# Kernel tuning notes

Measured on AMD Instinct MI355X. Metric: run time of the kernel, lower is better.

## Reference

```python
import jax, jax.numpy as jnp
import numpy as np

M = 128        # out_features (= in_features here)
N = 20000      # num_node
E = 320000     # num edges (avg degree 16)
KAPPA = 0.99   # inf-norm projection radius (A_rho = 1.0)


def project_linf(W, v):
    """Project each row of W onto the L1 ball of radius v (=> ||W||_inf <= v),
    matching IGNN's projection_norm_inf (rows with L1 norm <= v are untouched)."""
    absW = jnp.abs(W)
    row_l1 = absW.sum(axis=1)
    u = jnp.sort(absW, axis=1)[:, ::-1]          # descending per row
    cssv = jnp.cumsum(u, axis=1) - v
    ind = jnp.arange(1, W.shape[1] + 1, dtype=W.dtype)
    rho = jnp.sum(u * ind > cssv, axis=1)        # support size, >=1 when row_l1 > v
    theta = cssv[jnp.arange(W.shape[0]), rho - 1] / rho.astype(W.dtype)
    proj = jnp.sign(W) * jnp.maximum(absW - theta[:, None], 0.0)
    return jnp.where((row_l1 > v)[:, None], proj, W)


def spmm_right(Xm, rows, cols, vals, n):
    """Compute Xm @ A for sparse A with A[rows[e], cols[e]] = vals[e]; Xm: [m, n]."""
    g = Xm[:, rows] * vals                                    # [m, E]
    return jax.ops.segment_sum(g.T, cols, num_segments=n).T  # [m, n]


def setup_inputs() -> dict:
    key = jax.random.key(0)
    ks = jax.random.split(key, 7)
    stdv = 1.0 / np.sqrt(M)
    X_0 = jax.random.normal(ks[0], (M, N), jnp.float32)
    U = jax.random.normal(ks[1], (M, N), jnp.float32)
    W = jax.random.uniform(ks[2], (M, M), jnp.float32, -stdv, stdv)
    Omega_1 = jax.random.uniform(ks[3], (M, M), jnp.float32, -stdv, stdv)
    A_rows = jax.random.randint(ks[4], (E,), 0, N)
    A_cols = jax.random.randint(ks[5], (E,), 0, N)
    # positive, roughly degree-normalized adjacency values
    A_values = jax.random.uniform(ks[6], (E,), jnp.float32) / 16.0
    return dict(X_0=X_0, U=U, W=W, Omega_1=Omega_1, A_values=A_values,
                A_rows=A_rows, A_cols=A_cols, fw_mitr=30)


def reference(X_0, U, W, Omega_1, A_values, A_rows, A_cols, fw_mitr):
    n = X_0.shape[1]
    # self.W = projection_norm_inf(self.W, kappa / A_rho), A_rho = 1.0
    Wp = project_linf(W, KAPPA)
    # b_Omega = (A^T @ (U^T @ Omega_1^T))^T = (Omega_1 @ U) @ A
    B = spmm_right(Omega_1 @ U, A_rows, A_cols, A_values, n)  # [m, n]
    # ImplicitFunction fixed-point iteration: X <- phi(W @ X @ A + B), phi = relu
    def step(X, _):
        X_new = jax.nn.relu(spmm_right(Wp @ X, A_rows, A_cols, A_values, n) + B)
        return X_new, None
    X, _ = jax.lax.scan(step, X_0, None, length=fw_mitr)
    return X
```

## Files before the change

kernel.cpp:

```cpp
#include <hip/hip_runtime.h>

#define MDIM 128
#define NCOL 20000
#define NEDGE 320000
#define NITER 30
#define FKAPPA 0.99f

typedef unsigned int uint;
typedef unsigned short ushort;
typedef __attribute__((ext_vector_type(8))) short short8;
typedef __attribute__((ext_vector_type(4))) float f32x4;

__device__ __forceinline__ float bf2f(ushort b){
    uint u = ((uint)b) << 16;
    return __builtin_bit_cast(float, u);
}
__device__ __forceinline__ ushort f2bf(float f){
    uint u = __builtin_bit_cast(uint, f);
    uint r = (u + 0x7fffu + ((u >> 16) & 1u)) >> 16;
    return (ushort)r;
}

__global__ void k_zero(int* __restrict__ p){
    int i = blockIdx.x * 256 + threadIdx.x;
    if (i < 2 * NCOL) p[i] = 0;
}

__global__ void k_hist(const int* __restrict__ cols, int* __restrict__ cnt){
    int e = blockIdx.x * 256 + threadIdx.x;
    if (e < NEDGE) atomicAdd(&cnt[cols[e]], 1);
}

__global__ void k_scan(const int* __restrict__ cnt, int* __restrict__ start){
    __shared__ int lds[256];
    const int SEG = (NCOL + 255) / 256;
    int t = threadIdx.x;
    int lo = t * SEG;
    int hi = min(lo + SEG, NCOL);
    int s = 0;
    for (int i = lo; i < hi; ++i) s += cnt[i];
    lds[t] = s;
    __syncthreads();
    for (int off = 1; off < 256; off <<= 1){
        int v = (t >= off) ? lds[t - off] : 0;
        __syncthreads();
        lds[t] += v;
        __syncthreads();
    }
    int run = (t > 0) ? lds[t - 1] : 0;
    for (int i = lo; i < hi; ++i){ start[i] = run; run += cnt[i]; }
    if (hi == NCOL && lo < NCOL) start[NCOL] = run;
}

__global__ void k_scatter(const int* __restrict__ rows, const int* __restrict__ cols,
                          const float* __restrict__ vals, const int* __restrict__ start,
                          int* __restrict__ cursor, uint2* __restrict__ edges){
    int e = blockIdx.x * 256 + threadIdx.x;
    if (e < NEDGE){
        int c = cols[e];
        int p = start[c] + atomicAdd(&cursor[c], 1);
        edges[p] = make_uint2((uint)rows[e], __builtin_bit_cast(uint, vals[e]));
    }
}

__global__ void k_project(const float* __restrict__ W, ushort* __restrict__ Wp){
    int row = blockIdx.x * 4 + (threadIdx.x >> 6);
    int l = threadIdx.x & 63;
    const float* wr = W + row * MDIM;
    float w0 = wr[l], w1 = wr[l + 64];
    float a0 = fabsf(w0), a1 = fabsf(w1);
    float s = a0 + a1, mx = fmaxf(a0, a1);
    for (int off = 32; off; off >>= 1){
        s += __shfl_xor(s, off);
        mx = fmaxf(mx, __shfl_xor(mx, off));
    }
    if (s > FKAPPA){
        float tlo = 0.f, thi = mx;
        for (int it = 0; it < 48; ++it){
            float th = 0.5f * (tlo + thi);
            float f = fmaxf(a0 - th, 0.f) + fmaxf(a1 - th, 0.f);
            for (int off = 32; off; off >>= 1) f += __shfl_xor(f, off);
            if (f > FKAPPA) tlo = th; else thi = th;
        }
        float th = 0.5f * (tlo + thi);
        w0 = copysignf(fmaxf(a0 - th, 0.f), w0);
        w1 = copysignf(fmaxf(a1 - th, 0.f), w1);
    }
    Wp[row * MDIM + l] = f2bf(w0);
    Wp[row * MDIM + l + 64] = f2bf(w1);
}

__global__ void k_cvt(const float* __restrict__ src, ushort* __restrict__ dst){
    int i = blockIdx.x * 256 + threadIdx.x;
    if (i < MDIM * MDIM) dst[i] = f2bf(src[i]);
}

__global__ void k_tin(const float* __restrict__ X0, const float* __restrict__ U,
                      ushort* __restrict__ Xt, ushort* __restrict__ Ut){
    __shared__ ushort tile[128 * 66];
    const float* src = blockIdx.y ? U : X0;
    ushort* dst = blockIdx.y ? Ut : Xt;
    int c0 = blockIdx.x * 64;
    int t = threadIdx.x;
    for (int it = 0; it < 32; ++it){
        int le = it * 256 + t;
        int j = le & 63, m = le >> 6;
        int c = c0 + j;
        tile[m * 66 + j] = (c < NCOL) ? f2bf(src[m * NCOL + c]) : (ushort)0;
    }
    __syncthreads();
    for (int it = 0; it < 32; ++it){
        int le = it * 256 + t;
        int m = le & 127, jc = le >> 7;
        int c = c0 + jc;
        if (c < NCOL) dst[c * MDIM + m] = tile[m * 66 + jc];
    }
}

__global__ void k_tout(const ushort* __restrict__ Xt, float* __restrict__ out){
    __shared__ ushort tile[128 * 66];
    int c0 = blockIdx.x * 64;
    int t = threadIdx.x;
    for (int it = 0; it < 32; ++it){
        int le = it * 256 + t;
        int m = le & 127, jc = le >> 7;
        int c = c0 + jc;
        tile[m * 66 + jc] = (c < NCOL) ? Xt[c * MDIM + m] : (ushort)0;
    }
    __syncthreads();
    for (int it = 0; it < 32; ++it){
        int le = it * 256 + t;
        int j = le & 63, m = le >> 6;
        int c = c0 + j;
        if (c < NCOL) out[m * NCOL + c] = bf2f(tile[m * 66 + j]);
    }
}

__device__ __forceinline__ void fma8(float* acc, uint4 x, float v){
    acc[0] += v * bf2f((ushort)(x.x & 0xffffu)); acc[1] += v * bf2f((ushort)(x.x >> 16));
    acc[2] += v * bf2f((ushort)(x.y & 0xffffu)); acc[3] += v * bf2f((ushort)(x.y >> 16));
    acc[4] += v * bf2f((ushort)(x.z & 0xffffu)); acc[5] += v * bf2f((ushort)(x.z >> 16));
    acc[6] += v * bf2f((ushort)(x.w & 0xffffu)); acc[7] += v * bf2f((ushort)(x.w >> 16));
}

template<int MODE>
__global__ __launch_bounds__(256, 5) void k_fused(const ushort* __restrict__ Xt_in,
                        const ushort* __restrict__ Mat,
                        const ushort* __restrict__ Bt,
                        ushort* __restrict__ outp,
                        const int* __restrict__ start,
                        const uint2* __restrict__ edges){
    __shared__ alignas(16) char GL[4 * 1024];
    int t = threadIdx.x;
    int w = t >> 6, l = t & 63;
    int c0 = blockIdx.x * 16;
    int g = l >> 4;
    int sub = l & 15;

    int sa[5];
    #pragma unroll
    for (int i = 0; i < 5; ++i) sa[i] = start[c0 + w * 4 + i];

    uint2 myv[4];
    #pragma unroll
    for (int jj = 0; jj < 4; ++jj){
        int s = sa[jj], e = sa[jj + 1];
        int idx = (e > s) ? min(s + l, e - 1) : 0;
        myv[jj] = edges[idx];
    }

    #pragma unroll
    for (int jj = 0; jj < 4; ++jj){
        int s = sa[jj], e = sa[jj + 1];
        int d = e - s;
        float acc[8] = {0.f,0.f,0.f,0.f,0.f,0.f,0.f,0.f};
        if (d > 0){
            uint2 my = myv[jj];
            if (d <= 16){
                int r[4]; float v[4];
                #pragma unroll
                for (int b = 0; b < 4; ++b){
                    int slot = b * 4 + g;
                    int sel = min(slot, d - 1);
                    r[b] = __shfl((int)my.x, sel);
                    float vt = __builtin_bit_cast(float, __shfl((int)my.y, sel));
                    v[b] = (slot < d) ? vt : 0.f;
                }
                uint4 x[4];
                #pragma unroll
                for (int b = 0; b < 4; ++b)
                    x[b] = *(const uint4*)(Xt_in + (size_t)(uint)r[b] * 128 + sub * 8);
                #pragma unroll
                for (int b = 0; b < 4; ++b) fma8(acc, x[b], v[b]);
            } else {
                int r[8]; float v[8];
                #pragma unroll
                for (int b = 0; b < 8; ++b){
                    int slot = b * 4 + g;
                    int sel = min(slot, min(d, 64) - 1);
                    r[b] = __shfl((int)my.x, sel);
                    float vt = __builtin_bit_cast(float, __shfl((int)my.y, sel));
                    v[b] = (slot < d) ? vt : 0.f;
                }
                uint4 x[8];
                #pragma unroll
                for (int b = 0; b < 8; ++b)
                    x[b] = *(const uint4*)(Xt_in + (size_t)(uint)r[b] * 128 + sub * 8);
                #pragma unroll
                for (int b = 0; b < 8; ++b) fma8(acc, x[b], v[b]);
                if (d > 32){
                    for (int k2 = s + 32; k2 < e; k2 += 4){
                        int ke = k2 + g;
                        uint2 p = edges[min(ke, e - 1)];
                        float vv = (ke < e) ? __builtin_bit_cast(float, p.y) : 0.f;
                        uint4 xx = *(const uint4*)(Xt_in + (size_t)p.x * 128 + sub * 8);
                        fma8(acc, xx, vv);
                    }
                }
            }
        }
        #pragma unroll
        for (int i = 0; i < 8; ++i){
            acc[i] += __shfl_xor(acc[i], 16);
            acc[i] += __shfl_xor(acc[i], 32);
        }
        int j = w * 4 + jj;
        if (l < 16){
            uint4 pk;
            pk.x = (uint)f2bf(acc[0]) | ((uint)f2bf(acc[1]) << 16);
            pk.y = (uint)f2bf(acc[2]) | ((uint)f2bf(acc[3]) << 16);
            pk.z = (uint)f2bf(acc[4]) | ((uint)f2bf(acc[5]) << 16);
            pk.w = (uint)f2bf(acc[6]) | ((uint)f2bf(acc[7]) << 16);
            *(uint4*)(GL + ((j * 256 + sub * 16) ^ ((j & 7) << 4))) = pk;
        }
    }

    __builtin_amdgcn_sched_barrier(0);

    short8 bfr[2][4];
    #pragma unroll
    for (int mt = 0; mt < 2; ++mt){
        int m = w * 32 + mt * 16 + (l & 15);
        #pragma unroll
        for (int kc = 0; kc < 4; ++kc)
            bfr[mt][kc] = *(const short8*)(Mat + m * MDIM + kc * 32 + (l >> 4) * 8);
    }
    __syncthreads();

    {
        int arow = l & 15;
        int klane = (l >> 4) * 16;
        int asw = (arow & 7) << 4;
        short8 afr[4];
        #pragma unroll
        for (int kc = 0; kc < 4; ++kc)
            afr[kc] = *(const short8*)(GL + ((arow * 256 + kc * 64 + klane) ^ asw));
        #pragma unroll
        for (int mt = 0; mt < 2; ++mt){
            int m = w * 32 + mt * 16 + (l & 15);
            f32x4 acc4 = {0.f, 0.f, 0.f, 0.f};
            #pragma unroll
            for (int kc = 0; kc < 4; ++kc)
                acc4 = __builtin_amdgcn_mfma_f32_16x16x32_bf16(afr[kc], bfr[mt][kc], acc4, 0, 0, 0);
            int crow_base = c0 + ((l >> 4) << 2);
            #pragma unroll
            for (int q = 0; q < 4; ++q){
                int c = crow_base + q;
                float val = acc4[q];
                if (MODE == 1){
                    val += bf2f(Bt[c * MDIM + m]);
                    val = fmaxf(val, 0.f);
                }
                outp[c * MDIM + m] = f2bf(val);
            }
        }
    }
}

extern "C" void kernel_launch(void* const* d_in, const int* in_sizes, int n_in,
                              void* d_out, int out_size, void* d_ws, size_t ws_size,
                              hipStream_t stream){
    const float* X0 = (const float*)d_in[0];
    const float* U  = (const float*)d_in[1];
    const float* W  = (const float*)d_in[2];
    const float* Om = (const float*)d_in[3];
    const float* Av = (const float*)d_in[4];
    const int*   Ar = (const int*)d_in[5];
    const int*   Ac = (const int*)d_in[6];
    (void)in_sizes; (void)n_in; (void)out_size; (void)ws_size;

    char* ws = (char*)d_ws;
    size_t off = 0;
    auto alloc = [&](size_t bytes) -> char* {
        char* p = ws + off;
        off += (bytes + 255) & ~(size_t)255;
        return p;
    };
    int*    start = (int*)alloc((NCOL + 1) * 4);
    uint2*  edges = (uint2*)alloc(NEDGE * 8);
    ushort* Wp    = (ushort*)alloc(MDIM * MDIM * 2);
    ushort* Omb   = (ushort*)alloc(MDIM * MDIM * 2);
    ushort* P0    = (ushort*)alloc(NCOL * MDIM * 2);

    int* cnt    = (int*)P0;
    int* cursor = cnt + NCOL;

    ushort* P1   = (ushort*)d_out;
    ushort* BtBF = (ushort*)((char*)d_out + NCOL * MDIM * 2);

    k_zero<<<(2 * NCOL + 255) / 256, 256, 0, stream>>>(cnt);
    k_hist<<<(NEDGE + 255) / 256, 256, 0, stream>>>(Ac, cnt);
    k_scan<<<1, 256, 0, stream>>>(cnt, start);
    k_scatter<<<(NEDGE + 255) / 256, 256, 0, stream>>>(Ar, Ac, Av, start, cursor, edges);
    k_project<<<32, 256, 0, stream>>>(W, Wp);
    k_cvt<<<64, 256, 0, stream>>>(Om, Omb);
    k_tin<<<dim3(313, 2), 256, 0, stream>>>(X0, U, P0, P1);
    k_fused<0><<<1250, 256, 0, stream>>>(P1, Omb, nullptr, BtBF, start, edges);
    const ushort* cur = P0; ushort* nxt = P1;
    for (int i = 0; i < NITER; ++i){
        k_fused<1><<<1250, 256, 0, stream>>>(cur, Wp, BtBF, nxt, start, edges);
        ushort* tmp = (ushort*)cur; cur = nxt; nxt = tmp;
    }
    k_tout<<<313, 256, 0, stream>>>(cur, (float*)d_out);
}
```

Baseline: 592.0 us.

## Split fused gather+GEMM into separate dense GEMM then sparse gather kernels

Reorders each iteration from aggregate-then-multiply, (X@A) then W·, to multiply-then-aggregate, W·X then gather over A, using two kernels per iteration instead of one fused kernel. The gather kernel no longer needs LDS or a block barrier, so it can run at higher occupancy, and it applies the bias and ReLU with vectorized row loads. The cost is an extra Z buffer written and read from global memory on every iteration, plus twice as many kernel launches. The workspace layout also changes, with X, Z and B now living in the workspace instead of the output buffer.

Result: slower. 1.031 ms (+74.1%).

```diff
diff --git a/kernel.cpp b/kernel.cpp
--- a/kernel.cpp
+++ b/kernel.cpp
@@ -19,6 +19,9 @@
     uint u = __builtin_bit_cast(uint, f);
     uint r = (u + 0x7fffu + ((u >> 16) & 1u)) >> 16;
     return (ushort)r;
+}
+__device__ __forceinline__ uint pack2(float a, float b){
+    return (uint)f2bf(a) | ((uint)f2bf(b) << 16);
 }
 
 __global__ void k_zero(int* __restrict__ p){
@@ -143,14 +146,41 @@
     acc[6] += v * bf2f((ushort)(x.w & 0xffffu)); acc[7] += v * bf2f((ushort)(x.w >> 16));
 }
 
+__global__ __launch_bounds__(256, 4) void k_gemm(const ushort* __restrict__ Xt,
+                        const ushort* __restrict__ Mat, ushort* __restrict__ Zt){
+    int t = threadIdx.x;
+    int w = t >> 6, l = t & 63;
+    int c0 = blockIdx.x * 16;
+    short8 afr[4];
+    #pragma unroll
+    for (int kc = 0; kc < 4; ++kc)
+        afr[kc] = *(const short8*)(Xt + (size_t)(c0 + (l & 15)) * MDIM + kc * 32 + (l >> 4) * 8);
+    short8 bfr[2][4];
+    #pragma unroll
+    for (int mt = 0; mt < 2; ++mt){
+        int m = w * 32 + mt * 16 + (l & 15);
+        #pragma unroll
+        for (int kc = 0; kc < 4; ++kc)
+            bfr[mt][kc] = *(const short8*)(Mat + m * MDIM + kc * 32 + (l >> 4) * 8);
+    }
+    #pragma unroll
+    for (int mt = 0; mt < 2; ++mt){
+        int m = w * 32 + mt * 16 + (l & 15);
+        f32x4 a4 = {0.f, 0.f, 0.f, 0.f};
+        #pragma unroll
+        for (int kc = 0; kc < 4; ++kc)
+            a4 = __builtin_amdgcn_mfma_f32_16x16x32_bf16(afr[kc], bfr[mt][kc], a4, 0, 0, 0);
+        int cb = c0 + ((l >> 4) << 2);
+        #pragma unroll
+        for (int q = 0; q < 4; ++q)
+            Zt[(size_t)(cb + q) * MDIM + m] = f2bf(a4[q]);
+    }
+}
+
 template<int MODE>
-__global__ __launch_bounds__(256, 5) void k_fused(const ushort* __restrict__ Xt_in,
-                        const ushort* __restrict__ Mat,
-                        const ushort* __restrict__ Bt,
-                        ushort* __restrict__ outp,
-                        const int* __restrict__ start,
-                        const uint2* __restrict__ edges){
-    __shared__ alignas(16) char GL[4 * 1024];
+__global__ __launch_bounds__(256, 6) void k_gather(const ushort* __restrict__ Zt,
+                        const ushort* __restrict__ Bt, ushort* __restrict__ outp,
+                        const int* __restrict__ start, const uint2* __restrict__ edges){
     int t = threadIdx.x;
     int w = t >> 6, l = t & 63;
     int c0 = blockIdx.x * 16;
@@ -189,7 +219,7 @@
                 uint4 x[4];
                 #pragma unroll
                 for (int b = 0; b < 4; ++b)
-                    x[b] = *(const uint4*)(Xt_in + (size_t)(uint)r[b] * 128 + sub * 8);
+                    x[b] = *(const uint4*)(Zt + (size_t)(uint)r[b] * MDIM + sub * 8);
                 #pragma unroll
                 for (int b = 0; b < 4; ++b) fma8(acc, x[b], v[b]);
             } else {
@@ -205,7 +235,7 @@
                 uint4 x[8];
                 #pragma unroll
                 for (int b = 0; b < 8; ++b)
-                    x[b] = *(const uint4*)(Xt_in + (size_t)(uint)r[b] * 128 + sub * 8);
+                    x[b] = *(const uint4*)(Zt + (size_t)(uint)r[b] * MDIM + sub * 8);
                 #pragma unroll
                 for (int b = 0; b < 8; ++b) fma8(acc, x[b], v[b]);
                 if (d > 32){
@@ -213,7 +243,7 @@
                         int ke = k2 + g;
                         uint2 p = edges[min(ke, e - 1)];
                         float vv = (ke < e) ? __builtin_bit_cast(float, p.y) : 0.f;
-                        uint4 xx = *(const uint4*)(Xt_in + (size_t)p.x * 128 + sub * 8);
+                        uint4 xx = *(const uint4*)(Zt + (size_t)p.x * MDIM + sub * 8);
                         fma8(acc, xx, vv);
                     }
                 }
@@ -224,55 +254,26 @@
             acc[i] += __shfl_xor(acc[i], 16);
             acc[i] += __shfl_xor(acc[i], 32);
         }
-        int j = w * 4 + jj;
+        int c = c0 + w * 4 + jj;
         if (l < 16){
             uint4 pk;
-            pk.x = (uint)f2bf(acc[0]) | ((uint)f2bf(acc[1]) << 16);
-            pk.y = (uint)f2bf(acc[2]) | ((uint)f2bf(acc[3]) << 16);
-            pk.z = (uint)f2bf(acc[4]) | ((uint)f2bf(acc[5]) << 16);
-            pk.w = (uint)f2bf(acc[6]) | ((uint)f2bf(acc[7]) << 16);
-            *(uint4*)(GL + ((j * 256 + sub * 16) ^ ((j & 7) << 4))) = pk;
-        }
-    }
-
-    __builtin_amdgcn_sched_barrier(0);
-
-    short8 bfr[2][4];
-    #pragma unroll
-    for (int mt = 0; mt < 2; ++mt){
-        int m = w * 32 + mt * 16 + (l & 15);
-        #pragma unroll
-        for (int kc = 0; kc < 4; ++kc)
-            bfr[mt][kc] = *(const short8*)(Mat + m * MDIM + kc * 32 + (l >> 4) * 8);
-    }
-    __syncthreads();
-
-    {
-        int arow = l & 15;
-        int klane = (l >> 4) * 16;
-        int asw = (arow & 7) << 4;
-        short8 afr[4];
-        #pragma unroll
-        for (int kc = 0; kc < 4; ++kc)
-            afr[kc] = *(const short8*)(GL + ((arow * 256 + kc * 64 + klane) ^ asw));
-        #pragma unroll
-        for (int mt = 0; mt < 2; ++mt){
-            int m = w * 32 + mt * 16 + (l & 15);
-            f32x4 acc4 = {0.f, 0.f, 0.f, 0.f};
-            #pragma unroll
-            for (int kc = 0; kc < 4; ++kc)
-                acc4 = __builtin_amdgcn_mfma_f32_16x16x32_bf16(afr[kc], bfr[mt][kc], acc4, 0, 0, 0);
-            int crow_base = c0 + ((l >> 4) << 2);
-            #pragma unroll
-            for (int q = 0; q < 4; ++q){
-                int c = crow_base + q;
-                float val = acc4[q];
-                if (MODE == 1){
-                    val += bf2f(Bt[c * MDIM + m]);
-                    val = fmaxf(val, 0.f);
-                }
-                outp[c * MDIM + m] = f2bf(val);
+            if (MODE == 1){
+                uint4 bt = *(const uint4*)(Bt + (size_t)c * MDIM + sub * 8);
+                pk.x = pack2(fmaxf(acc[0] + bf2f((ushort)(bt.x & 0xffffu)), 0.f),
+                             fmaxf(acc[1] + bf2f((ushort)(bt.x >> 16)), 0.f));
+                pk.y = pack2(fmaxf(acc[2] + bf2f((ushort)(bt.y & 0xffffu)), 0.f),
+                             fmaxf(acc[3] + bf2f((ushort)(bt.y >> 16)), 0.f));
+                pk.z = pack2(fmaxf(acc[4] + bf2f((ushort)(bt.z & 0xffffu)), 0.f),
+                             fmaxf(acc[5] + bf2f((ushort)(bt.z >> 16)), 0.f));
+                pk.w = pack2(fmaxf(acc[6] + bf2f((ushort)(bt.w & 0xffffu)), 0.f),
+                             fmaxf(acc[7] + bf2f((ushort)(bt.w >> 16)), 0.f));
+            } else {
+                pk.x = pack2(acc[0], acc[1]);
+                pk.y = pack2(acc[2], acc[3]);
+                pk.z = pack2(acc[4], acc[5]);
+                pk.w = pack2(acc[6], acc[7]);
             }
+            *(uint4*)(outp + (size_t)c * MDIM + sub * 8) = pk;
         }
     }
 }
@@ -300,13 +301,14 @@
     uint2*  edges = (uint2*)alloc(NEDGE * 8);
     ushort* Wp    = (ushort*)alloc(MDIM * MDIM * 2);
     ushort* Omb   = (ushort*)alloc(MDIM * MDIM * 2);
-    ushort* P0    = (ushort*)alloc(NCOL * MDIM * 2);
-
-    int* cnt    = (int*)P0;
+    ushort* Xb    = (ushort*)alloc(NCOL * MDIM * 2);
+    ushort* Z     = (ushort*)alloc(NCOL * MDIM * 2);
+    ushort* BtBF  = (ushort*)alloc(NCOL * MDIM * 2);
+
+    int* cnt    = (int*)Z;
     int* cursor = cnt + NCOL;
 
-    ushort* P1   = (ushort*)d_out;
-    ushort* BtBF = (ushort*)((char*)d_out + NCOL * MDIM * 2);
+    ushort* Ut = (ushort*)d_out;
 
     k_zero<<<(2 * NCOL + 255) / 256, 256, 0, stream>>>(cnt);
     k_hist<<<(NEDGE + 255) / 256, 256, 0, stream>>>(Ac, cnt);
@@ -314,12 +316,14 @@
     k_scatter<<<(NEDGE + 255) / 256, 256, 0, stream>>>(Ar, Ac, Av, start, cursor, edges);
     k_project<<<32, 256, 0, stream>>>(W, Wp);
     k_cvt<<<64, 256, 0, stream>>>(Om, Omb);
-    k_tin<<<dim3(313, 2), 256, 0, stream>>>(X0, U, P0, P1);
-    k_fused<0><<<1250, 256, 0, stream>>>(P1, Omb, nullptr, BtBF, start, edges);
-    const ushort* cur = P0; ushort* nxt = P1;
+    k_tin<<<dim3(313, 2), 256, 0, stream>>>(X0, U, Xb, Ut);
+
+    k_gemm<<<1250, 256, 0, stream>>>(Ut, Omb, Z);
+    k_gather<0><<<1250, 256, 0, stream>>>(Z, nullptr, BtBF, start, edges);
+
     for (int i = 0; i < NITER; ++i){
-        k_fused<1><<<1250, 256, 0, stream>>>(cur, Wp, BtBF, nxt, start, edges);
-        ushort* tmp = (ushort*)cur; cur = nxt; nxt = tmp;
-    }
-    k_tout<<<313, 256, 0, stream>>>(cur, (float*)d_out);
-}
+        k_gemm<<<1250, 256, 0, stream>>>(Xb, Wp, Z);
+        k_gather<1><<<1250, 256, 0, stream>>>(Z, BtBF, Xb, start, edges);
+    }
+    k_tout<<<313, 256, 0, stream>>>(Xb, (float*)d_out);
+}
```
